# Optimization experiments

Measured on AMD Instinct MI355X. Metric: run time of the kernel, lower is better.

Reference implementation:

```python
import jax, jax.numpy as jnp
import numpy as np

B, T, C, H = 256, 256, 384, 64  # batch, seq (== block_size), n_embd, head_size


def setup_inputs() -> dict:
    key = jax.random.key(0)
    kx, kk, kq, kv = jax.random.split(key, 4)
    scale = C ** -0.5
    x = jax.random.normal(kx, (B, T, C), dtype=jnp.float32)
    Wk = jax.random.normal(kk, (C, H), dtype=jnp.float32) * scale
    Wq = jax.random.normal(kq, (C, H), dtype=jnp.float32) * scale
    Wv = jax.random.normal(kv, (C, H), dtype=jnp.float32) * scale
    return {"x": x, "Wk": Wk, "Wq": Wq, "Wv": Wv}


def reference(x, Wk, Wq, Wv):
    # Single causal self-attention head (x_kv=None path). Dropout is eval-mode (identity).
    Tn = x.shape[1]
    k = x @ Wk            # [B, T, H]
    q = x @ Wq            # [B, T, H]
    v = x @ Wv            # [B, T, H]
    inv_sqrt_d = k.shape[-1] ** -0.5
    wei = jnp.einsum('bth,bsh->bts', q, k) * inv_sqrt_d  # [B, T, T]
    causal = jnp.tril(jnp.ones((Tn, Tn), dtype=bool))
    wei = jnp.where(causal, wei, -jnp.inf)
    wei = jax.nn.softmax(wei, axis=-1)
    out = jnp.einsum('bts,bsh->bth', wei, v)             # [B, T, H]
    return out
```

## Files before the change

### kernel.cpp

```cpp
#include <hip/hip_runtime.h>

#define BATCH 256
#define SEQ   256
#define CDIM  384
#define HDIM  64

typedef __attribute__((ext_vector_type(8))) short bf16x8;
typedef __attribute__((ext_vector_type(4))) float f32x4;

__device__ __forceinline__ unsigned f2bf(float f) {
  union { float f; unsigned u; } v; v.f = f;
  unsigned r = v.u + 0x7FFFu + ((v.u >> 16) & 1u);
  return r >> 16;
}

__global__ void wtrans_kernel(const float* __restrict__ Wk, const float* __restrict__ Wq,
                              const float* __restrict__ Wv, unsigned short* __restrict__ WTf) {
  int gid = blockIdx.x * 256 + threadIdx.x;
  if (gid >= 192 * CDIM) return;
  int n = gid / CDIM, kk = gid - n * CDIM;
  const float* W = (n < 64) ? Wq : (n < 128) ? Wk : Wv;
  int nt = n >> 4, ln = n & 15, ks = kk >> 5, sub = (kk >> 3) & 3, j = kk & 7;
  int lane = ln + 16 * sub;
  WTf[(((size_t)ks * 12 + nt) * 64 + lane) * 8 + j] =
      (unsigned short)f2bf(W[kk * HDIM + (n & 63)]);
}

__global__ __launch_bounds__(1024, 4) void fused_kernel(
    const float* __restrict__ x, const unsigned short* __restrict__ WTf,
    float* __restrict__ out) {
  __shared__ __align__(16) unsigned short lds[73728];
  const int tid = threadIdx.x, b = blockIdx.x;
  const int w = tid >> 6, lane = tid & 63;
  const int ln15 = lane & 15, quad = lane >> 4;

  {
    const uint4* src = (const uint4*)WTf;
    #pragma unroll
    for (int i = 0; i < 9; ++i) {
      int c = i * 1024 + tid;
      __builtin_amdgcn_global_load_lds(
          (const __attribute__((address_space(1))) unsigned*)(src + c),
          (__attribute__((address_space(3))) unsigned*)((char*)lds + (size_t)c * 16),
          16, 0, 0);
    }
  }
  __builtin_amdgcn_sched_barrier(0);

  const float* xr = x + (size_t)(b * 256 + w * 16 + ln15) * CDIM + quad * 8;

  float4 P0[6], P1[6];

#define LOADST(BUF, BASE)                                                    \
  {                                                                          \
    _Pragma("unroll")                                                        \
    for (int j = 0; j < 3; ++j) {                                            \
      BUF[2 * j]     = *(const float4*)(xr + (BASE + j) * 32);               \
      BUF[2 * j + 1] = *(const float4*)(xr + (BASE + j) * 32 + 4);           \
    }                                                                        \
  }

#define USEST(BUF, BASE)                                                     \
  {                                                                          \
    _Pragma("unroll")                                                        \
    for (int k2 = 0; k2 < 3; ++k2) {                                         \
      float4 a0 = BUF[2 * k2], a1 = BUF[2 * k2 + 1];                         \
      bf16x8 t;                                                              \
      t[0] = (short)f2bf(a0.x); t[1] = (short)f2bf(a0.y);                    \
      t[2] = (short)f2bf(a0.z); t[3] = (short)f2bf(a0.w);                    \
      t[4] = (short)f2bf(a1.x); t[5] = (short)f2bf(a1.y);                    \
      t[6] = (short)f2bf(a1.z); t[7] = (short)f2bf(a1.w);                    \
      _Pragma("unroll")                                                      \
      for (int nt = 0; nt < 12; ++nt) {                                      \
        bf16x8 aw = *(const bf16x8*)&lds[(((BASE + k2) * 12 + nt) * 64 + lane) * 8]; \
        acc[nt] = __builtin_amdgcn_mfma_f32_16x16x32_bf16(aw, t, acc[nt], 0, 0, 0);  \
      }                                                                      \
    }                                                                        \
  }

  LOADST(P0, 0)
  __builtin_amdgcn_sched_barrier(0);

  asm volatile("s_waitcnt vmcnt(6)" ::: "memory");
  __builtin_amdgcn_s_barrier();
  __builtin_amdgcn_sched_barrier(0);

  f32x4 acc[12];
  #pragma unroll
  for (int nt = 0; nt < 12; ++nt) acc[nt] = (f32x4){0.f, 0.f, 0.f, 0.f};

  LOADST(P1, 3)
  USEST(P0, 0)
  LOADST(P0, 6)
  USEST(P1, 3)
  LOADST(P1, 9)
  USEST(P0, 6)
  USEST(P1, 9)

  __syncthreads();

  unsigned short (*QL)[72]  = (unsigned short(*)[72])lds;
  unsigned short (*KL)[72]  = (unsigned short(*)[72])(lds + 18432);
  unsigned short (*VT)[264] = (unsigned short(*)[264])(lds + 36864);
  unsigned short (*PL)[36]  = (unsigned short(*)[36])(lds + 53760 + w * 576);

  {
    const int trow = w * 16 + ln15;
    #pragma unroll
    for (int nt = 0; nt < 4; ++nt) {
      f32x4 a = acc[nt];
      unsigned p0 = f2bf(a[0]) | (f2bf(a[1]) << 16);
      unsigned p1 = f2bf(a[2]) | (f2bf(a[3]) << 16);
      *(uint2*)&QL[trow][nt * 16 + quad * 4] = (uint2){p0, p1};
    }
    #pragma unroll
    for (int nt = 4; nt < 8; ++nt) {
      f32x4 a = acc[nt];
      unsigned p0 = f2bf(a[0]) | (f2bf(a[1]) << 16);
      unsigned p1 = f2bf(a[2]) | (f2bf(a[3]) << 16);
      *(uint2*)&KL[trow][(nt - 4) * 16 + quad * 4] = (uint2){p0, p1};
    }
    #pragma unroll
    for (int nt = 8; nt < 12; ++nt) {
      f32x4 a = acc[nt];
      const int h = (nt - 8) * 16 + quad * 4;
      #pragma unroll
      for (int i = 0; i < 4; ++i)
        VT[h + i][trow] = (unsigned short)f2bf(a[i]);
    }
  }
  __syncthreads();

  {
    const int mt = w;
    const int t0 = mt * 16;
    const int NT = (mt | 1) + 1;

    bf16x8 aq[2];
    #pragma unroll
    for (int ks = 0; ks < 2; ++ks)
      aq[ks] = *(const bf16x8*)&QL[t0 + ln15][ks * 32 + quad * 8];

    float sv[16][4];
    #pragma unroll
    for (int nt = 0; nt < 16; ++nt) {
      if (nt < NT) {
        f32x4 a2 = (f32x4){0.f, 0.f, 0.f, 0.f};
        #pragma unroll
        for (int ks = 0; ks < 2; ++ks) {
          bf16x8 bf = *(const bf16x8*)&KL[nt * 16 + ln15][ks * 32 + quad * 8];
          a2 = __builtin_amdgcn_mfma_f32_16x16x32_bf16(aq[ks], bf, a2, 0, 0, 0);
        }
        int colg = nt * 16 + ln15;
        #pragma unroll
        for (int i = 0; i < 4; ++i) {
          int rowg = t0 + quad * 4 + i;
          sv[nt][i] = (colg <= rowg) ? a2[i] * 0.125f : -3.0e38f;
        }
      }
    }
    float mx[4] = {-3.0e38f, -3.0e38f, -3.0e38f, -3.0e38f};
    #pragma unroll
    for (int nt = 0; nt < 16; ++nt)
      if (nt < NT) {
        #pragma unroll
        for (int i = 0; i < 4; ++i) mx[i] = fmaxf(mx[i], sv[nt][i]);
      }
    #pragma unroll
    for (int i = 0; i < 4; ++i) {
      mx[i] = fmaxf(mx[i], __shfl_xor(mx[i], 8, 64));
      mx[i] = fmaxf(mx[i], __shfl_xor(mx[i], 4, 64));
      mx[i] = fmaxf(mx[i], __shfl_xor(mx[i], 2, 64));
      mx[i] = fmaxf(mx[i], __shfl_xor(mx[i], 1, 64));
    }
    float sm[4] = {0.f, 0.f, 0.f, 0.f};
    #pragma unroll
    for (int nt = 0; nt < 16; ++nt)
      if (nt < NT) {
        #pragma unroll
        for (int i = 0; i < 4; ++i) {
          float e = __expf(sv[nt][i] - mx[i]);
          sv[nt][i] = e;
          sm[i] += e;
        }
      }
    #pragma unroll
    for (int i = 0; i < 4; ++i) {
      sm[i] += __shfl_xor(sm[i], 8, 64);
      sm[i] += __shfl_xor(sm[i], 4, 64);
      sm[i] += __shfl_xor(sm[i], 2, 64);
      sm[i] += __shfl_xor(sm[i], 1, 64);
    }
    float inv[4];
    #pragma unroll
    for (int i = 0; i < 4; ++i) inv[i] = 1.0f / sm[i];

    f32x4 o[4];
    #pragma unroll
    for (int ont = 0; ont < 4; ++ont) o[ont] = (f32x4){0.f, 0.f, 0.f, 0.f};

    #pragma unroll
    for (int kc = 0; kc < 8; ++kc) {
      if (kc * 2 < NT) {
        #pragma unroll
        for (int half = 0; half < 2; ++half) {
          int nt = kc * 2 + half;
          #pragma unroll
          for (int i = 0; i < 4; ++i)
            PL[quad * 4 + i][half * 16 + ln15] =
                (unsigned short)f2bf(sv[nt][i] * inv[i]);
        }
        bf16x8 pa = *(const bf16x8*)&PL[ln15][quad * 8];
        #pragma unroll
        for (int ont = 0; ont < 4; ++ont) {
          bf16x8 vb = *(const bf16x8*)&VT[ont * 16 + ln15][kc * 32 + quad * 8];
          o[ont] = __builtin_amdgcn_mfma_f32_16x16x32_bf16(pa, vb, o[ont], 0, 0, 0);
        }
      }
    }

    #pragma unroll
    for (int ont = 0; ont < 4; ++ont) {
      int h = ont * 16 + ln15;
      #pragma unroll
      for (int i = 0; i < 4; ++i)
        out[(size_t)(b * 256 + t0 + quad * 4 + i) * HDIM + h] = o[ont][i];
    }
  }
}

extern "C" void kernel_launch(void* const* d_in, const int* in_sizes, int n_in,
                              void* d_out, int out_size, void* d_ws, size_t ws_size,
                              hipStream_t stream) {
  const float* x  = (const float*)d_in[0];
  const float* Wk = (const float*)d_in[1];
  const float* Wq = (const float*)d_in[2];
  const float* Wv = (const float*)d_in[3];
  float* out = (float*)d_out;

  unsigned short* WTf = (unsigned short*)d_ws;

  wtrans_kernel<<<(192 * CDIM + 255) / 256, 256, 0, stream>>>(Wk, Wq, Wv, WTf);
  fused_kernel<<<256, 1024, 0, stream>>>(x, WTf, out);
}
```

Before: 169.8 us.

## Halve block size to 512 threads, two row tiles per wave

Each block now runs 8 waves instead of 16. In the projection, each wave computes two 16-row tiles, so one LDS weight fragment feeds two MFMAs. In the attention phase, each wave handles a light causal tile (w) and its heavy mirror (15-w) to balance work across waves. The aim is to halve the LDS weight reads per MFMA and even out causal imbalance. The cost is more registers per thread (two accumulator sets, larger prefetch buffers) and less parallelism per block.

```diff
diff --git a/kernel.cpp b/kernel.cpp
--- a/kernel.cpp
+++ b/kernel.cpp
@@ -26,7 +26,7 @@
       (unsigned short)f2bf(W[kk * HDIM + (n & 63)]);
 }
 
-__global__ __launch_bounds__(1024, 4) void fused_kernel(
+__global__ __launch_bounds__(512, 2) void fused_kernel(
     const float* __restrict__ x, const unsigned short* __restrict__ WTf,
     float* __restrict__ out) {
   __shared__ __align__(16) unsigned short lds[73728];
@@ -35,28 +35,29 @@
   const int ln15 = lane & 15, quad = lane >> 4;
 
   {
-    const uint4* src = (const uint4*)WTf;
-    #pragma unroll
-    for (int i = 0; i < 9; ++i) {
-      int c = i * 1024 + tid;
+    #pragma unroll
+    for (int i = 0; i < 18; ++i) {
+      int c = i * 512 + tid;
       __builtin_amdgcn_global_load_lds(
-          (const __attribute__((address_space(1))) unsigned*)(src + c),
+          (const __attribute__((address_space(1))) unsigned*)((const char*)WTf + (size_t)c * 16),
           (__attribute__((address_space(3))) unsigned*)((char*)lds + (size_t)c * 16),
           16, 0, 0);
     }
   }
   __builtin_amdgcn_sched_barrier(0);
 
-  const float* xr = x + (size_t)(b * 256 + w * 16 + ln15) * CDIM + quad * 8;
-
-  float4 P0[6], P1[6];
+  const float* xr = x + (size_t)(b * 256 + w * 32 + ln15) * CDIM + quad * 8;
+
+  float4 P0[12], P1[12];
 
 #define LOADST(BUF, BASE)                                                    \
   {                                                                          \
     _Pragma("unroll")                                                        \
     for (int j = 0; j < 3; ++j) {                                            \
-      BUF[2 * j]     = *(const float4*)(xr + (BASE + j) * 32);               \
-      BUF[2 * j + 1] = *(const float4*)(xr + (BASE + j) * 32 + 4);           \
+      BUF[4 * j]     = *(const float4*)(xr + ((BASE) + j) * 32);             \
+      BUF[4 * j + 1] = *(const float4*)(xr + ((BASE) + j) * 32 + 4);         \
+      BUF[4 * j + 2] = *(const float4*)(xr + 16 * CDIM + ((BASE) + j) * 32); \
+      BUF[4 * j + 3] = *(const float4*)(xr + 16 * CDIM + ((BASE) + j) * 32 + 4); \
     }                                                                        \
   }
 
@@ -64,16 +65,22 @@
   {                                                                          \
     _Pragma("unroll")                                                        \
     for (int k2 = 0; k2 < 3; ++k2) {                                         \
-      float4 a0 = BUF[2 * k2], a1 = BUF[2 * k2 + 1];                         \
-      bf16x8 t;                                                              \
-      t[0] = (short)f2bf(a0.x); t[1] = (short)f2bf(a0.y);                    \
-      t[2] = (short)f2bf(a0.z); t[3] = (short)f2bf(a0.w);                    \
-      t[4] = (short)f2bf(a1.x); t[5] = (short)f2bf(a1.y);                    \
-      t[6] = (short)f2bf(a1.z); t[7] = (short)f2bf(a1.w);                    \
+      float4 a0 = BUF[4 * k2],     a1 = BUF[4 * k2 + 1];                     \
+      float4 c0 = BUF[4 * k2 + 2], c1 = BUF[4 * k2 + 3];                     \
+      bf16x8 t0, t1;                                                         \
+      t0[0] = (short)f2bf(a0.x); t0[1] = (short)f2bf(a0.y);                  \
+      t0[2] = (short)f2bf(a0.z); t0[3] = (short)f2bf(a0.w);                  \
+      t0[4] = (short)f2bf(a1.x); t0[5] = (short)f2bf(a1.y);                  \
+      t0[6] = (short)f2bf(a1.z); t0[7] = (short)f2bf(a1.w);                  \
+      t1[0] = (short)f2bf(c0.x); t1[1] = (short)f2bf(c0.y);                  \
+      t1[2] = (short)f2bf(c0.z); t1[3] = (short)f2bf(c0.w);                  \
+      t1[4] = (short)f2bf(c1.x); t1[5] = (short)f2bf(c1.y);                  \
+      t1[6] = (short)f2bf(c1.z); t1[7] = (short)f2bf(c1.w);                  \
       _Pragma("unroll")                                                      \
       for (int nt = 0; nt < 12; ++nt) {                                      \
-        bf16x8 aw = *(const bf16x8*)&lds[(((BASE + k2) * 12 + nt) * 64 + lane) * 8]; \
-        acc[nt] = __builtin_amdgcn_mfma_f32_16x16x32_bf16(aw, t, acc[nt], 0, 0, 0);  \
+        bf16x8 aw = *(const bf16x8*)&lds[((((BASE) + k2) * 12 + nt) * 64 + lane) * 8]; \
+        acc0[nt] = __builtin_amdgcn_mfma_f32_16x16x32_bf16(aw, t0, acc0[nt], 0, 0, 0); \
+        acc1[nt] = __builtin_amdgcn_mfma_f32_16x16x32_bf16(aw, t1, acc1[nt], 0, 0, 0); \
       }                                                                      \
     }                                                                        \
   }
@@ -81,13 +88,16 @@
   LOADST(P0, 0)
   __builtin_amdgcn_sched_barrier(0);
 
-  asm volatile("s_waitcnt vmcnt(6)" ::: "memory");
+  asm volatile("s_waitcnt vmcnt(12)" ::: "memory");
   __builtin_amdgcn_s_barrier();
   __builtin_amdgcn_sched_barrier(0);
 
-  f32x4 acc[12];
+  f32x4 acc0[12], acc1[12];
   #pragma unroll
-  for (int nt = 0; nt < 12; ++nt) acc[nt] = (f32x4){0.f, 0.f, 0.f, 0.f};
+  for (int nt = 0; nt < 12; ++nt) {
+    acc0[nt] = (f32x4){0.f, 0.f, 0.f, 0.f};
+    acc1[nt] = (f32x4){0.f, 0.f, 0.f, 0.f};
+  }
 
   LOADST(P1, 3)
   USEST(P0, 0)
@@ -104,35 +114,42 @@
   unsigned short (*VT)[264] = (unsigned short(*)[264])(lds + 36864);
   unsigned short (*PL)[36]  = (unsigned short(*)[36])(lds + 53760 + w * 576);
 
+#define HANDOFF(ACC, TROW)                                                   \
+  {                                                                          \
+    _Pragma("unroll")                                                        \
+    for (int nt = 0; nt < 4; ++nt) {                                         \
+      f32x4 a = ACC[nt];                                                     \
+      unsigned p0 = f2bf(a[0]) | (f2bf(a[1]) << 16);                         \
+      unsigned p1 = f2bf(a[2]) | (f2bf(a[3]) << 16);                         \
+      *(uint2*)&QL[TROW][nt * 16 + quad * 4] = (uint2){p0, p1};              \
+    }                                                                        \
+    _Pragma("unroll")                                                        \
+    for (int nt = 4; nt < 8; ++nt) {                                         \
+      f32x4 a = ACC[nt];                                                     \
+      unsigned p0 = f2bf(a[0]) | (f2bf(a[1]) << 16);                         \
+      unsigned p1 = f2bf(a[2]) | (f2bf(a[3]) << 16);                         \
+      *(uint2*)&KL[TROW][(nt - 4) * 16 + quad * 4] = (uint2){p0, p1};        \
+    }                                                                        \
+    _Pragma("unroll")                                                        \
+    for (int nt = 8; nt < 12; ++nt) {                                        \
+      f32x4 a = ACC[nt];                                                     \
+      const int h = (nt - 8) * 16 + quad * 4;                                \
+      _Pragma("unroll")                                                      \
+      for (int i = 0; i < 4; ++i)                                            \
+        VT[h + i][TROW] = (unsigned short)f2bf(a[i]);                        \
+    }                                                                        \
+  }
+
   {
-    const int trow = w * 16 + ln15;
-    #pragma unroll
-    for (int nt = 0; nt < 4; ++nt) {
-      f32x4 a = acc[nt];
-      unsigned p0 = f2bf(a[0]) | (f2bf(a[1]) << 16);
-      unsigned p1 = f2bf(a[2]) | (f2bf(a[3]) << 16);
-      *(uint2*)&QL[trow][nt * 16 + quad * 4] = (uint2){p0, p1};
-    }
-    #pragma unroll
-    for (int nt = 4; nt < 8; ++nt) {
-      f32x4 a = acc[nt];
-      unsigned p0 = f2bf(a[0]) | (f2bf(a[1]) << 16);
-      unsigned p1 = f2bf(a[2]) | (f2bf(a[3]) << 16);
-      *(uint2*)&KL[trow][(nt - 4) * 16 + quad * 4] = (uint2){p0, p1};
-    }
-    #pragma unroll
-    for (int nt = 8; nt < 12; ++nt) {
-      f32x4 a = acc[nt];
-      const int h = (nt - 8) * 16 + quad * 4;
-      #pragma unroll
-      for (int i = 0; i < 4; ++i)
-        VT[h + i][trow] = (unsigned short)f2bf(a[i]);
-    }
+    const int trow0 = w * 32 + ln15;
+    const int trow1 = trow0 + 16;
+    HANDOFF(acc0, trow0)
+    HANDOFF(acc1, trow1)
   }
   __syncthreads();
 
-  {
-    const int mt = w;
+  for (int mi = 0; mi < 2; ++mi) {
+    const int mt = mi ? (15 - w) : w;
     const int t0 = mt * 16;
     const int NT = (mt | 1) + 1;
 
@@ -241,5 +258,5 @@
   unsigned short* WTf = (unsigned short*)d_ws;
 
   wtrans_kernel<<<(192 * CDIM + 255) / 256, 256, 0, stream>>>(Wk, Wq, Wv, WTf);
-  fused_kernel<<<256, 1024, 0, stream>>>(x, WTf, out);
-}
+  fused_kernel<<<256, 512, 0, stream>>>(x, WTf, out);
+}
```

Result: no change. 172.5 us (+1.5%).

## Balance causal attention work across waves by splitting long rows and dropping max pass

Applied to the files above, without the earlier changes.

Rebalances the causal triangle: each wave handles at most 10 key tiles for its own query tile, and waves 0-5 also compute the tail key tiles (10..15) for the mirrored long query tiles 10-15. They pass partial outputs and row sums to the owning waves through LDS for a final merge. Softmax drops the row-max subtraction and normalizes after PV, removing a reduction pass. The no-max exp risks overflow for larger logits, and the extra barrier and LDS exchange add some overhead.

```diff
diff --git a/kernel.cpp b/kernel.cpp
--- a/kernel.cpp
+++ b/kernel.cpp
@@ -132,99 +132,138 @@
   __syncthreads();
 
   {
-    const int mt = w;
-    const int t0 = mt * 16;
-    const int NT = (mt | 1) + 1;
-
-    bf16x8 aq[2];
-    #pragma unroll
-    for (int ks = 0; ks < 2; ++ks)
-      aq[ks] = *(const bf16x8*)&QL[t0 + ln15][ks * 32 + quad * 8];
-
-    float sv[16][4];
-    #pragma unroll
-    for (int nt = 0; nt < 16; ++nt) {
-      if (nt < NT) {
-        f32x4 a2 = (f32x4){0.f, 0.f, 0.f, 0.f};
+    const int uo = (w | 1) + 1;
+    const int nA = (uo < 10) ? uo : 10;
+    const int mtB = 15 - w;
+    const int nB = (w < 6) ? (((mtB | 1) + 1) - 10) : 0;
+
+    bf16x8 aqA[2], aqB[2];
+    #pragma unroll
+    for (int ks = 0; ks < 2; ++ks) {
+      aqA[ks] = *(const bf16x8*)&QL[w * 16 + ln15][ks * 32 + quad * 8];
+      aqB[ks] = *(const bf16x8*)&QL[mtB * 16 + ln15][ks * 32 + quad * 8];
+    }
+    asm volatile("s_waitcnt lgkmcnt(0)" ::: "memory");
+    __builtin_amdgcn_s_barrier();
+    __builtin_amdgcn_sched_barrier(0);
+
+    float* PB = (float*)lds;
+
+    float sv[10][4];
+    float sm[4] = {0.f, 0.f, 0.f, 0.f};
+    f32x4 o[4];
+    #pragma unroll
+    for (int t = 0; t < 4; ++t) o[t] = (f32x4){0.f, 0.f, 0.f, 0.f};
+
+#define AJOB(AQ, MT, N0, CNT)                                                 \
+    {                                                                         \
+      _Pragma("unroll")                                                       \
+      for (int j = 0; j < 10; ++j) {                                          \
+        if (j < (CNT)) {                                                      \
+          const int nt = (N0) + j;                                            \
+          f32x4 a2 = (f32x4){0.f, 0.f, 0.f, 0.f};                             \
+          _Pragma("unroll")                                                   \
+          for (int ks = 0; ks < 2; ++ks) {                                    \
+            bf16x8 bf = *(const bf16x8*)&KL[nt * 16 + ln15][ks * 32 + quad * 8]; \
+            a2 = __builtin_amdgcn_mfma_f32_16x16x32_bf16((AQ)[ks], bf, a2, 0, 0, 0); \
+          }                                                                   \
+          const int colg = nt * 16 + ln15;                                    \
+          _Pragma("unroll")                                                   \
+          for (int i = 0; i < 4; ++i) {                                       \
+            const int rowg = (MT) * 16 + quad * 4 + i;                        \
+            float e = (colg <= rowg) ? __expf(a2[i] * 0.125f) : 0.f;          \
+            sv[j][i] = e;                                                     \
+            sm[i] += e;                                                       \
+          }                                                                   \
+        }                                                                     \
+      }                                                                       \
+      _Pragma("unroll")                                                       \
+      for (int kc = 0; kc < 5; ++kc) {                                        \
+        if (kc * 2 < (CNT)) {                                                 \
+          _Pragma("unroll")                                                   \
+          for (int half = 0; half < 2; ++half) {                              \
+            _Pragma("unroll")                                                 \
+            for (int i = 0; i < 4; ++i)                                       \
+              PL[quad * 4 + i][half * 16 + ln15] =                            \
+                  (unsigned short)f2bf(sv[kc * 2 + half][i]);                 \
+          }                                                                   \
+          bf16x8 pa = *(const bf16x8*)&PL[ln15][quad * 8];                    \
+          _Pragma("unroll")                                                   \
+          for (int ont = 0; ont < 4; ++ont) {                                 \
+            bf16x8 vb = *(const bf16x8*)&VT[ont * 16 + ln15][((N0) + kc * 2) * 16 + quad * 8]; \
+            o[ont] = __builtin_amdgcn_mfma_f32_16x16x32_bf16(pa, vb, o[ont], 0, 0, 0); \
+          }                                                                   \
+        }                                                                     \
+      }                                                                       \
+    }
+
+    if (w < 6) {
+      AJOB(aqB, mtB, 10, nB)
+      float* slot = PB + (mtB - 10) * 1280;
+      #pragma unroll
+      for (int ont = 0; ont < 4; ++ont)
+        *(f32x4*)(slot + lane * 16 + ont * 4) = o[ont];
+      *(f32x4*)(slot + 1024 + lane * 4) = (f32x4){sm[0], sm[1], sm[2], sm[3]};
+      #pragma unroll
+      for (int i = 0; i < 4; ++i) sm[i] = 0.f;
+      #pragma unroll
+      for (int t = 0; t < 4; ++t) o[t] = (f32x4){0.f, 0.f, 0.f, 0.f};
+    }
+
+    AJOB(aqA, w, 0, nA)
+
+    if (w < 10) {
+      #pragma unroll
+      for (int i = 0; i < 4; ++i) {
+        sm[i] += __shfl_xor(sm[i], 8, 64);
+        sm[i] += __shfl_xor(sm[i], 4, 64);
+        sm[i] += __shfl_xor(sm[i], 2, 64);
+        sm[i] += __shfl_xor(sm[i], 1, 64);
+      }
+      float inv[4];
+      #pragma unroll
+      for (int i = 0; i < 4; ++i) inv[i] = 1.0f / sm[i];
+      #pragma unroll
+      for (int ont = 0; ont < 4; ++ont) {
+        int h = ont * 16 + ln15;
         #pragma unroll
-        for (int ks = 0; ks < 2; ++ks) {
-          bf16x8 bf = *(const bf16x8*)&KL[nt * 16 + ln15][ks * 32 + quad * 8];
-          a2 = __builtin_amdgcn_mfma_f32_16x16x32_bf16(aq[ks], bf, a2, 0, 0, 0);
-        }
-        int colg = nt * 16 + ln15;
+        for (int i = 0; i < 4; ++i)
+          out[(size_t)(b * 256 + w * 16 + quad * 4 + i) * HDIM + h] = o[ont][i] * inv[i];
+      }
+    }
+
+    asm volatile("s_waitcnt lgkmcnt(0)" ::: "memory");
+    __builtin_amdgcn_s_barrier();
+    __builtin_amdgcn_sched_barrier(0);
+
+    if (w >= 10) {
+      float* slot = PB + (w - 10) * 1280;
+      #pragma unroll
+      for (int ont = 0; ont < 4; ++ont) {
+        f32x4 po = *(const f32x4*)(slot + lane * 16 + ont * 4);
         #pragma unroll
-        for (int i = 0; i < 4; ++i) {
-          int rowg = t0 + quad * 4 + i;
-          sv[nt][i] = (colg <= rowg) ? a2[i] * 0.125f : -3.0e38f;
-        }
-      }
-    }
-    float mx[4] = {-3.0e38f, -3.0e38f, -3.0e38f, -3.0e38f};
-    #pragma unroll
-    for (int nt = 0; nt < 16; ++nt)
-      if (nt < NT) {
+        for (int i = 0; i < 4; ++i) o[ont][i] += po[i];
+      }
+      f32x4 ps = *(const f32x4*)(slot + 1024 + lane * 4);
+      #pragma unroll
+      for (int i = 0; i < 4; ++i) sm[i] += ps[i];
+      #pragma unroll
+      for (int i = 0; i < 4; ++i) {
+        sm[i] += __shfl_xor(sm[i], 8, 64);
+        sm[i] += __shfl_xor(sm[i], 4, 64);
+        sm[i] += __shfl_xor(sm[i], 2, 64);
+        sm[i] += __shfl_xor(sm[i], 1, 64);
+      }
+      float inv[4];
+      #pragma unroll
+      for (int i = 0; i < 4; ++i) inv[i] = 1.0f / sm[i];
+      #pragma unroll
+      for (int ont = 0; ont < 4; ++ont) {
+        int h = ont * 16 + ln15;
         #pragma unroll
-        for (int i = 0; i < 4; ++i) mx[i] = fmaxf(mx[i], sv[nt][i]);
-      }
-    #pragma unroll
-    for (int i = 0; i < 4; ++i) {
-      mx[i] = fmaxf(mx[i], __shfl_xor(mx[i], 8, 64));
-      mx[i] = fmaxf(mx[i], __shfl_xor(mx[i], 4, 64));
-      mx[i] = fmaxf(mx[i], __shfl_xor(mx[i], 2, 64));
-      mx[i] = fmaxf(mx[i], __shfl_xor(mx[i], 1, 64));
-    }
-    float sm[4] = {0.f, 0.f, 0.f, 0.f};
-    #pragma unroll
-    for (int nt = 0; nt < 16; ++nt)
-      if (nt < NT) {
-        #pragma unroll
-        for (int i = 0; i < 4; ++i) {
-          float e = __expf(sv[nt][i] - mx[i]);
-          sv[nt][i] = e;
-          sm[i] += e;
-        }
-      }
-    #pragma unroll
-    for (int i = 0; i < 4; ++i) {
-      sm[i] += __shfl_xor(sm[i], 8, 64);
-      sm[i] += __shfl_xor(sm[i], 4, 64);
-      sm[i] += __shfl_xor(sm[i], 2, 64);
-      sm[i] += __shfl_xor(sm[i], 1, 64);
-    }
-    float inv[4];
-    #pragma unroll
-    for (int i = 0; i < 4; ++i) inv[i] = 1.0f / sm[i];
-
-    f32x4 o[4];
-    #pragma unroll
-    for (int ont = 0; ont < 4; ++ont) o[ont] = (f32x4){0.f, 0.f, 0.f, 0.f};
-
-    #pragma unroll
-    for (int kc = 0; kc < 8; ++kc) {
-      if (kc * 2 < NT) {
-        #pragma unroll
-        for (int half = 0; half < 2; ++half) {
-          int nt = kc * 2 + half;
-          #pragma unroll
-          for (int i = 0; i < 4; ++i)
-            PL[quad * 4 + i][half * 16 + ln15] =
-                (unsigned short)f2bf(sv[nt][i] * inv[i]);
-        }
-        bf16x8 pa = *(const bf16x8*)&PL[ln15][quad * 8];
-        #pragma unroll
-        for (int ont = 0; ont < 4; ++ont) {
-          bf16x8 vb = *(const bf16x8*)&VT[ont * 16 + ln15][kc * 32 + quad * 8];
-          o[ont] = __builtin_amdgcn_mfma_f32_16x16x32_bf16(pa, vb, o[ont], 0, 0, 0);
-        }
-      }
-    }
-
-    #pragma unroll
-    for (int ont = 0; ont < 4; ++ont) {
-      int h = ont * 16 + ln15;
-      #pragma unroll
-      for (int i = 0; i < 4; ++i)
-        out[(size_t)(b * 256 + t0 + quad * 4 + i) * HDIM + h] = o[ont][i];
+        for (int i = 0; i < 4; ++i)
+          out[(size_t)(b * 256 + w * 16 + quad * 4 + i) * HDIM + h] = o[ont][i] * inv[i];
+      }
     }
   }
 }
```

After: 169.5 us (median of 2 runs). Within noise of the previous version (-0.2%).
